# Kernel optimization log

Measured on AMD Instinct MI355X. Metric: run time of the kernel, lower is better.

The kernel has to match this reference:

```python
import jax, jax.numpy as jnp
import numpy as np

N_GAUSS = 1536
WIDTH, HEIGHT = 160, 128
FX = FY = 146.44        # 2343.024 * (160/2560)
CX, CY = WIDTH / 2.0, HEIGHT / 2.0
EPS2D = 0.3             # 2D covariance dilation (as in prepare_rasterization_coefficients)
NEAR, FAR = 0.01, 1e10


def eval_sh_basis(dirs):
    # real SH basis up to degree 3, 16 components (matches eval_sh_old)
    x, y, z = dirs[..., 0], dirs[..., 1], dirs[..., 2]
    one = jnp.ones_like(x)
    return jnp.stack([
        0.282095 * one,
        -0.488603 * y, 0.488603 * z, -0.488603 * x,
        1.092548 * x * y, -1.092548 * y * z, 0.315392 * (3 * z * z - 1),
        -1.092548 * x * z, 0.546274 * (x * x - y * y),
        -0.590044 * y * (3 * x * x - y * y), 2.890611 * x * y * z,
        -0.457046 * y * (5 * z * z - 1), 0.373176 * z * (5 * z * z - 3),
        -0.457046 * x * (5 * z * z - 1), 1.445306 * z * (x * x - y * y),
        -0.590044 * x * (x * x - 3 * y * y)], axis=-1)


def quat_to_rot(q):
    q = q / jnp.linalg.norm(q, axis=1, keepdims=True)
    w, x, y, z = q[:, 0], q[:, 1], q[:, 2], q[:, 3]
    R = jnp.stack([
        1 - 2 * (y * y + z * z), 2 * (x * y - z * w), 2 * (x * z + y * w),
        2 * (x * y + z * w), 1 - 2 * (x * x + z * z), 2 * (y * z - x * w),
        2 * (x * z - y * w), 2 * (y * z + x * w), 1 - 2 * (x * x + y * y)], axis=-1)
    return R.reshape(-1, 3, 3)


def get_viewmat(c2w):
    # c2w: (B,3,4); flip y/z camera axes then invert (matches torch get_viewmat)
    R = c2w[:, :3, :3] * jnp.array([[[1.0, -1.0, -1.0]]], dtype=c2w.dtype)
    t = c2w[:, :3, 3:4]
    R_inv = jnp.swapaxes(R, 1, 2)
    t_inv = -(R_inv @ t)
    return R_inv[0], t_inv[0, :, 0]


def setup_inputs() -> dict:
    key = jax.random.key(0)
    k0, k1, k2, k3, k4, k5 = jax.random.split(key, 6)
    N = N_GAUSS
    xy = jax.random.normal(k0, (N, 2), dtype=jnp.float32) * 0.5
    # world z negative -> positive camera-frame depth after axis flip
    z = -(1.0 + 4.0 * jax.random.uniform(k1, (N, 1), dtype=jnp.float32))
    means = jnp.concatenate([xy, z], axis=1)
    quats = jax.random.normal(k2, (N, 4), dtype=jnp.float32)
    log_scales = jax.random.normal(k3, (N, 3), dtype=jnp.float32) * 0.3 - 3.0
    opacity_logits = jax.random.normal(k4, (N,), dtype=jnp.float32)
    sh_coeffs = jax.random.normal(k5, (N, 16, 3), dtype=jnp.float32) * 0.3
    camera_to_worlds = jnp.eye(4, dtype=jnp.float32)[None, :3, :]
    return {"means": means, "quats": quats, "log_scales": log_scales,
            "opacity_logits": opacity_logits, "sh_coeffs": sh_coeffs,
            "camera_to_worlds": camera_to_worlds}


def reference(means, quats, log_scales, opacity_logits, sh_coeffs, camera_to_worlds):
    R_w2c, t_w2c = get_viewmat(camera_to_worlds)
    means_cam = means @ R_w2c.T + t_w2c                    # (N,3)
    depth = means_cam[:, 2]
    mask = (depth > NEAR) & (depth < FAR)

    # view-dependent colors from SH (degree 3)
    cam_pos = camera_to_worlds[0, :3, 3]
    dirs = means - cam_pos
    dirs = dirs / jnp.linalg.norm(dirs, axis=1, keepdims=True)
    colors = jnp.maximum(jnp.einsum('nk,nkc->nc', eval_sh_basis(dirs), sh_coeffs) + 0.5, 0.0)

    # 3D covariance -> camera frame -> EWA 2D projection
    Rg = quat_to_rot(quats)                                 # (N,3,3)
    M = Rg * jnp.exp(log_scales)[:, None, :]                # R @ diag(S)
    cov3d = M @ jnp.swapaxes(M, 1, 2)
    cov_cam = jnp.einsum('ij,njk,lk->nil', R_w2c, cov3d, R_w2c)
    tx, ty, tz = means_cam[:, 0], means_cam[:, 1], means_cam[:, 2]
    rz = 1.0 / tz
    zero = jnp.zeros_like(rz)
    J = jnp.stack([jnp.stack([FX * rz, zero, -FX * tx * rz * rz], -1),
                   jnp.stack([zero, FY * rz, -FY * ty * rz * rz], -1)], -2)  # (N,2,3)
    cov2d = jnp.einsum('nij,njk,nlk->nil', J, cov_cam, J)
    a = cov2d[:, 0, 0] + EPS2D
    c = cov2d[:, 1, 1] + EPS2D
    b = cov2d[:, 0, 1]
    det = a * c - b * b
    A, B, C = c / det, -b / det, a / det                    # conic (inverse 2D cov)

    u = FX * tx * rz + CX
    v = FY * ty * rz + CY
    opac = jax.nn.sigmoid(opacity_logits)

    px = jnp.arange(WIDTH, dtype=means.dtype)
    py = jnp.arange(HEIGHT, dtype=means.dtype)
    dx = px[None, None, :] - u[:, None, None]               # (N,1,W)
    dy = py[None, :, None] - v[:, None, None]               # (N,H,1)
    power = (-0.5 * (A[:, None, None] * dx * dx + C[:, None, None] * dy * dy)
             - B[:, None, None] * (dx * dy))                # (N,H,W)
    alpha = jnp.minimum(0.999, opac[:, None, None] * jnp.exp(power))
    alpha = jnp.where(mask[:, None, None], alpha, 0.0)

    # global depth sort (front-to-back alpha compositing)
    order = jnp.argsort(jnp.where(mask, depth, jnp.inf))
    alpha = alpha[order]
    colors = colors[order]
    T = jnp.cumprod(1.0 - alpha, axis=0)
    T_excl = jnp.concatenate([jnp.ones_like(T[:1]), T[:-1]], axis=0)
    w = T_excl * alpha                                      # (N,H,W)
    rgb = jnp.einsum('nhw,nc->hwc', w, colors)              # (H,W,3)
    return rgb
```

## Files before the change

### kernel.cpp

```cpp
#include <hip/hip_runtime.h>
#include <math.h>

#define N_GAUSS 1536
#define WIDTH   160
#define HEIGHT  128
#define NPIX    (WIDTH * HEIGHT)
#define FXC     146.44f
#define FYC     146.44f
#define CXC     80.0f
#define CYC     64.0f
#define EPS2D   0.3f
#define NEARP   0.01f
#define FARP    1e10f
#define REC     12
#define L2E     1.4426950408889634f

#define PREP_BLOCKS 384
#define PREP_TPB    256
#define SCAN_LEN4   (N_GAUSS / 64 / 4)

#define NWAVE   16
#define RCHUNK  (N_GAUSS / NWAVE)
#define RPIX    64

__device__ __forceinline__ float fast_exp2(float x) {
    return __builtin_amdgcn_exp2f(x);
}


__global__ __launch_bounds__(PREP_TPB) void prep_sort_kernel(
    const float* __restrict__ means, const float* __restrict__ quats,
    const float* __restrict__ log_scales, const float* __restrict__ opac_logits,
    const float* __restrict__ sh, const float* __restrict__ c2w,
    float* __restrict__ sorted)
{
    __shared__ float4 k4_lds[N_GAUSS / 4];
    float* k_lds = (float*)k4_lds;

    float C[12];
#pragma unroll
    for (int k = 0; k < 12; k++) C[k] = c2w[k];
    float R00 =  C[0], R01 =  C[4], R02 =  C[8];
    float R10 = -C[1], R11 = -C[5], R12 = -C[9];
    float R20 = -C[2], R21 = -C[6], R22 = -C[10];
    float cpx = C[3], cpy = C[7], cpz = C[11];
    float t0 = -(R00 * cpx + R01 * cpy + R02 * cpz);
    float t1 = -(R10 * cpx + R11 * cpy + R12 * cpz);
    float t2 = -(R20 * cpx + R21 * cpy + R22 * cpz);

    for (int j = threadIdx.x; j < N_GAUSS; j += PREP_TPB) {
        float mx = means[3 * j], my = means[3 * j + 1], mz = means[3 * j + 2];
        float tzj = R20 * mx + R21 * my + R22 * mz + t2;
        bool m = (tzj > NEARP) && (tzj < FARP);
        k_lds[j] = m ? tzj : INFINITY;
    }
    __syncthreads();

    int i    = blockIdx.x * 4 + (threadIdx.x >> 6);
    int part = threadIdx.x & 63;

    float mx = means[3 * i], my = means[3 * i + 1], mz = means[3 * i + 2];
    float4 qv = ((const float4*)quats)[i];
    float lsx = log_scales[3 * i + 0];
    float lsy = log_scales[3 * i + 1];
    float lsz = log_scales[3 * i + 2];
    float olog = opac_logits[i];
    const float4* sh4 = (const float4*)(sh + i * 48);
    float4 S[12];
#pragma unroll
    for (int k = 0; k < 12; k++) S[k] = sh4[k];
    const float* shf = (const float*)S;

    float tx = R00 * mx + R01 * my + R02 * mz + t0;
    float ty = R10 * mx + R11 * my + R12 * mz + t1;
    float tz = R20 * mx + R21 * my + R22 * mz + t2;
    bool mask = (tz > NEARP) && (tz < FARP);

    float dx = mx - cpx, dy = my - cpy, dz = mz - cpz;
    float rn = rsqrtf(dx * dx + dy * dy + dz * dz);
    float x = dx * rn, y = dy * rn, z = dz * rn;
    float xx = x * x, yy = y * y, zz = z * z;
    float basis[16];
    basis[0]  = 0.282095f;
    basis[1]  = -0.488603f * y;
    basis[2]  = 0.488603f * z;
    basis[3]  = -0.488603f * x;
    basis[4]  = 1.092548f * x * y;
    basis[5]  = -1.092548f * y * z;
    basis[6]  = 0.315392f * (3.f * zz - 1.f);
    basis[7]  = -1.092548f * x * z;
    basis[8]  = 0.546274f * (xx - yy);
    basis[9]  = -0.590044f * y * (3.f * xx - yy);
    basis[10] = 2.890611f * x * y * z;
    basis[11] = -0.457046f * y * (5.f * zz - 1.f);
    basis[12] = 0.373176f * z * (5.f * zz - 3.f);
    basis[13] = -0.457046f * x * (5.f * zz - 1.f);
    basis[14] = 1.445306f * z * (xx - yy);
    basis[15] = -0.590044f * x * (xx - 3.f * yy);
    float cr = 0.f, cg = 0.f, cb = 0.f;
#pragma unroll
    for (int k = 0; k < 16; k++) {
        cr += basis[k] * shf[3 * k + 0];
        cg += basis[k] * shf[3 * k + 1];
        cb += basis[k] * shf[3 * k + 2];
    }
    cr = fmaxf(cr + 0.5f, 0.f);
    cg = fmaxf(cg + 0.5f, 0.f);
    cb = fmaxf(cb + 0.5f, 0.f);

    float qw = qv.x, qx = qv.y, qy = qv.z, qz = qv.w;
    float qn = rsqrtf(qw * qw + qx * qx + qy * qy + qz * qz);
    qw *= qn; qx *= qn; qy *= qn; qz *= qn;
    float sx = expf(lsx);
    float sy = expf(lsy);
    float sz = expf(lsz);
    float M00 = (1.f - 2.f * (qy * qy + qz * qz)) * sx;
    float M01 = (2.f * (qx * qy - qz * qw)) * sy;
    float M02 = (2.f * (qx * qz + qy * qw)) * sz;
    float M10 = (2.f * (qx * qy + qz * qw)) * sx;
    float M11 = (1.f - 2.f * (qx * qx + qz * qz)) * sy;
    float M12 = (2.f * (qy * qz - qx * qw)) * sz;
    float M20 = (2.f * (qx * qz - qy * qw)) * sx;
    float M21 = (2.f * (qy * qz + qx * qw)) * sy;
    float M22 = (1.f - 2.f * (qx * qx + qy * qy)) * sz;
    float V00 = M00 * M00 + M01 * M01 + M02 * M02;
    float V01 = M00 * M10 + M01 * M11 + M02 * M12;
    float V02 = M00 * M20 + M01 * M21 + M02 * M22;
    float V11 = M10 * M10 + M11 * M11 + M12 * M12;
    float V12 = M10 * M20 + M11 * M21 + M12 * M22;
    float V22 = M20 * M20 + M21 * M21 + M22 * M22;

    float T00 = R00 * V00 + R01 * V01 + R02 * V02;
    float T01 = R00 * V01 + R01 * V11 + R02 * V12;
    float T02 = R00 * V02 + R01 * V12 + R02 * V22;
    float T10 = R10 * V00 + R11 * V01 + R12 * V02;
    float T11 = R10 * V01 + R11 * V11 + R12 * V12;
    float T12 = R10 * V02 + R11 * V12 + R12 * V22;
    float T20 = R20 * V00 + R21 * V01 + R22 * V02;
    float T21 = R20 * V01 + R21 * V11 + R22 * V12;
    float T22 = R20 * V02 + R21 * V12 + R22 * V22;
    float cc00 = T00 * R00 + T01 * R01 + T02 * R02;
    float cc01 = T00 * R10 + T01 * R11 + T02 * R12;
    float cc02 = T00 * R20 + T01 * R21 + T02 * R22;
    float cc11 = T10 * R10 + T11 * R11 + T12 * R12;
    float cc12 = T10 * R20 + T11 * R21 + T12 * R22;
    float cc22 = T20 * R20 + T21 * R21 + T22 * R22;

    float rz = 1.f / tz;
    float rz2 = rz * rz;
    float j00 = FXC * rz, j02 = -FXC * tx * rz2;
    float j11 = FYC * rz, j12 = -FYC * ty * rz2;
    float c2d00 = j00 * j00 * cc00 + 2.f * j00 * j02 * cc02 + j02 * j02 * cc22;
    float c2d01 = (j00 * cc01 + j02 * cc12) * j11 + (j00 * cc02 + j02 * cc22) * j12;
    float c2d11 = j11 * j11 * cc11 + 2.f * j11 * j12 * cc12 + j12 * j12 * cc22;

    float a = c2d00 + EPS2D, c = c2d11 + EPS2D, b = c2d01;
    float idet = 1.f / (a * c - b * b);
    float Ac = c * idet, Bc = -b * idet, Cc = a * idet;
    float u = FXC * tx * rz + CXC;
    float v = FYC * ty * rz + CYC;
    float op = 1.f / (1.f + expf(-olog));
    float a2 = -0.5f * L2E * Ac;
    float b2 = -L2E * Bc;
    float c2 = -0.5f * L2E * Cc;
    float o2 = log2f(op);
    if (!mask) {
        u = 0.f; v = 0.f; a2 = 0.f; b2 = 0.f; c2 = 0.f; o2 = -INFINITY;
    }

    float ki = k_lds[i];
    int rank = 0;
    int base4 = part * SCAN_LEN4;
#pragma unroll
    for (int jj = 0; jj < SCAN_LEN4; jj++) {
        int j4 = base4 + jj;
        float4 kk = k4_lds[j4];
        int j = 4 * j4;
        rank += (kk.x < ki) || (kk.x == ki && (j + 0) < i);
        rank += (kk.y < ki) || (kk.y == ki && (j + 1) < i);
        rank += (kk.z < ki) || (kk.z == ki && (j + 2) < i);
        rank += (kk.w < ki) || (kk.w == ki && (j + 3) < i);
    }
    rank += __shfl_xor(rank, 1);
    rank += __shfl_xor(rank, 2);
    rank += __shfl_xor(rank, 4);
    rank += __shfl_xor(rank, 8);
    rank += __shfl_xor(rank, 16);
    rank += __shfl_xor(rank, 32);

    if (part == 0) {
        float4* dst = (float4*)(sorted + rank * REC);
        dst[0] = make_float4(u, v, a2, b2);
        dst[1] = make_float4(c2, o2, cr, cg);
        dst[2] = make_float4(cb, 0.f, 0.f, 0.f);
    }
}

__global__ __launch_bounds__(1024) void raster_kernel(
    const float4* __restrict__ sorted4, float* __restrict__ out)
{
    __shared__ float4 part_lds[NWAVE * RPIX];

    int wave = __builtin_amdgcn_readfirstlane(threadIdx.x >> 6);
    int lane = threadIdx.x & 63;
    int p = blockIdx.x * RPIX + lane;
    float px = (float)(p % WIDTH);
    float py = (float)(p / WIDTH);

    const float4* src = sorted4 + wave * (RCHUNK * 3);

    float T = 1.f, cr = 0.f, cg = 0.f, cb = 0.f;
#pragma unroll 4
    for (int j = 0; j < RCHUNK; j++) {
        float4 f0 = src[3 * j + 0];
        float4 f1 = src[3 * j + 1];
        float4 f2 = src[3 * j + 2];
        float dx = px - f0.x;
        float dy = py - f0.y;
        float t  = f0.z * dx;
        t = fmaf(f0.w, dy, t);
        float q  = f1.x * dy;
        float pw = fmaf(t, dx, f1.y);
        pw = fmaf(q, dy, pw);
        float alpha = fminf(0.999f, fast_exp2(pw));
        float w = T * alpha;
        cr = fmaf(w, f1.z, cr);
        cg = fmaf(w, f1.w, cg);
        cb = fmaf(w, f2.x, cb);
        T -= w;
    }
    part_lds[wave * RPIX + lane] = make_float4(cr, cg, cb, T);
    __syncthreads();

    if (threadIdx.x < RPIX) {
        int pp = blockIdx.x * RPIX + threadIdx.x;
        float Tt = 1.f, r = 0.f, g = 0.f, b = 0.f;
#pragma unroll
        for (int c = 0; c < NWAVE; c++) {
            float4 q = part_lds[c * RPIX + threadIdx.x];
            r = fmaf(Tt, q.x, r);
            g = fmaf(Tt, q.y, g);
            b = fmaf(Tt, q.z, b);
            Tt *= q.w;
        }
        out[3 * pp + 0] = r;
        out[3 * pp + 1] = g;
        out[3 * pp + 2] = b;
    }
}

extern "C" void kernel_launch(void* const* d_in, const int* in_sizes, int n_in,
                              void* d_out, int out_size, void* d_ws, size_t ws_size,
                              hipStream_t stream) {
    const float* means       = (const float*)d_in[0];
    const float* quats       = (const float*)d_in[1];
    const float* log_scales  = (const float*)d_in[2];
    const float* opac_logits = (const float*)d_in[3];
    const float* sh          = (const float*)d_in[4];
    const float* c2w         = (const float*)d_in[5];

    float* ws     = (float*)d_ws;
    float* sorted = ws;

    prep_sort_kernel<<<PREP_BLOCKS, PREP_TPB, 0, stream>>>(
        means, quats, log_scales, opac_logits, sh, c2w, sorted);
    raster_kernel<<<NPIX / RPIX, NWAVE * 64, 0, stream>>>(
        (const float4*)sorted, (float*)d_out);
}
```

Baseline: 87.90 us.

## Cull Gaussians per 8x8 tile using screen-space bounding boxes

The prep kernel now emits a per-Gaussian bounding box (center plus radii at which the opacity-weighted Gaussian falls below exp(-25)) alongside a reorganized record layout. The raster kernel switches from linear 64-pixel strips to 8x8 tiles. Each wave ballots which of its Gaussians overlap the tile and only evaluates those, skipping the exp and blend for distant splats. This drops contributions below the exp(-25) cutoff, which is a small approximation to the reference. It also adds ballot/shuffle overhead and divergent loop trip counts.

```diff
diff --git a/kernel.cpp b/kernel.cpp
--- a/kernel.cpp
+++ b/kernel.cpp
@@ -12,8 +12,9 @@
 #define EPS2D   0.3f
 #define NEARP   0.01f
 #define FARP    1e10f
-#define REC     12
 #define L2E     1.4426950408889634f
+#define LN2     0.6931471805599453f
+#define CULL_E  25.0f
 
 #define PREP_BLOCKS 384
 #define PREP_TPB    256
@@ -22,6 +23,10 @@
 #define NWAVE   16
 #define RCHUNK  (N_GAUSS / NWAVE)
 #define RPIX    64
+#define TILE_W  8
+#define TILE_H  8
+#define TILES_X (WIDTH / TILE_W)
+#define TILES_Y (HEIGHT / TILE_H)
 
 __device__ __forceinline__ float fast_exp2(float x) {
     return __builtin_amdgcn_exp2f(x);
@@ -32,7 +37,7 @@
     const float* __restrict__ means, const float* __restrict__ quats,
     const float* __restrict__ log_scales, const float* __restrict__ opac_logits,
     const float* __restrict__ sh, const float* __restrict__ c2w,
-    float* __restrict__ sorted)
+    float4* __restrict__ bbox, float4* __restrict__ rec)
 {
     __shared__ float4 k4_lds[N_GAUSS / 4];
     float* k_lds = (float*)k4_lds;
@@ -164,8 +169,14 @@
     float b2 = -L2E * Bc;
     float c2 = -0.5f * L2E * Cc;
     float o2 = log2f(op);
+
+    float Qmax = fmaxf(0.f, 2.f * LN2 * (CULL_E + o2));
+    float rx = sqrtf(Qmax * a);
+    float ry = sqrtf(Qmax * c);
+
     if (!mask) {
-        u = 0.f; v = 0.f; a2 = 0.f; b2 = 0.f; c2 = 0.f; o2 = -INFINITY;
+        u = 1e30f; v = 1e30f; rx = 0.f; ry = 0.f;
+        a2 = 0.f; b2 = 0.f; c2 = 0.f; o2 = -INFINITY;
     }
 
     float ki = k_lds[i];
@@ -189,63 +200,82 @@
     rank += __shfl_xor(rank, 32);
 
     if (part == 0) {
-        float4* dst = (float4*)(sorted + rank * REC);
-        dst[0] = make_float4(u, v, a2, b2);
-        dst[1] = make_float4(c2, o2, cr, cg);
-        dst[2] = make_float4(cb, 0.f, 0.f, 0.f);
+        bbox[rank]        = make_float4(u, v, rx, ry);
+        rec[2 * rank]     = make_float4(a2, b2, c2, o2);
+        rec[2 * rank + 1] = make_float4(cr, cg, cb, 0.f);
     }
 }
 
 __global__ __launch_bounds__(1024) void raster_kernel(
-    const float4* __restrict__ sorted4, float* __restrict__ out)
+    const float4* __restrict__ bbox, const float4* __restrict__ rec,
+    float* __restrict__ out)
 {
     __shared__ float4 part_lds[NWAVE * RPIX];
 
     int wave = __builtin_amdgcn_readfirstlane(threadIdx.x >> 6);
     int lane = threadIdx.x & 63;
-    int p = blockIdx.x * RPIX + lane;
-    float px = (float)(p % WIDTH);
-    float py = (float)(p / WIDTH);
-
-    const float4* src = sorted4 + wave * (RCHUNK * 3);
+
+    int tile = blockIdx.x;
+    int tx0 = (tile % TILES_X) * TILE_W;
+    int ty0 = (tile / TILES_X) * TILE_H;
+    float px = (float)(tx0 + (lane & 7));
+    float py = (float)(ty0 + (lane >> 3));
+    float tcx = (float)tx0 + 3.5f;
+    float tcy = (float)ty0 + 3.5f;
+
+    int g0 = wave * RCHUNK;
 
     float T = 1.f, cr = 0.f, cg = 0.f, cb = 0.f;
-#pragma unroll 4
-    for (int j = 0; j < RCHUNK; j++) {
-        float4 f0 = src[3 * j + 0];
-        float4 f1 = src[3 * j + 1];
-        float4 f2 = src[3 * j + 2];
-        float dx = px - f0.x;
-        float dy = py - f0.y;
-        float t  = f0.z * dx;
-        t = fmaf(f0.w, dy, t);
-        float q  = f1.x * dy;
-        float pw = fmaf(t, dx, f1.y);
-        pw = fmaf(q, dy, pw);
-        float alpha = fminf(0.999f, fast_exp2(pw));
-        float w = T * alpha;
-        cr = fmaf(w, f1.z, cr);
-        cg = fmaf(w, f1.w, cg);
-        cb = fmaf(w, f2.x, cb);
-        T -= w;
+#pragma unroll
+    for (int bseg = 0; bseg < 2; bseg++) {
+        int gbase = g0 + (bseg ? 64 : 0);
+        int bn    = bseg ? 32 : 64;
+        float4 bb = bbox[gbase + (lane < bn ? lane : 0)];
+        bool ok = (lane < bn) &&
+                  (fabsf(tcx - bb.x) <= bb.z + 3.5f) &&
+                  (fabsf(tcy - bb.y) <= bb.w + 3.5f);
+        unsigned long long m = __ballot(ok);
+        while (m) {
+            int bl = __ffsll(m) - 1;
+            m &= m - 1;
+            float u = __shfl(bb.x, bl);
+            float v = __shfl(bb.y, bl);
+            int g = gbase + bl;
+            float4 f1 = rec[2 * g];
+            float4 f2 = rec[2 * g + 1];
+            float dx = px - u;
+            float dy = py - v;
+            float t  = f1.x * dx;
+            t = fmaf(f1.y, dy, t);
+            float q  = f1.z * dy;
+            float pw = fmaf(t, dx, f1.w);
+            pw = fmaf(q, dy, pw);
+            float alpha = fminf(0.999f, fast_exp2(pw));
+            float w = T * alpha;
+            cr = fmaf(w, f2.x, cr);
+            cg = fmaf(w, f2.y, cg);
+            cb = fmaf(w, f2.z, cb);
+            T -= w;
+        }
     }
     part_lds[wave * RPIX + lane] = make_float4(cr, cg, cb, T);
     __syncthreads();
 
     if (threadIdx.x < RPIX) {
-        int pp = blockIdx.x * RPIX + threadIdx.x;
+        int l = threadIdx.x;
+        int p = (ty0 + (l >> 3)) * WIDTH + tx0 + (l & 7);
         float Tt = 1.f, r = 0.f, g = 0.f, b = 0.f;
 #pragma unroll
         for (int c = 0; c < NWAVE; c++) {
-            float4 q = part_lds[c * RPIX + threadIdx.x];
+            float4 q = part_lds[c * RPIX + l];
             r = fmaf(Tt, q.x, r);
             g = fmaf(Tt, q.y, g);
             b = fmaf(Tt, q.z, b);
             Tt *= q.w;
         }
-        out[3 * pp + 0] = r;
-        out[3 * pp + 1] = g;
-        out[3 * pp + 2] = b;
+        out[3 * p + 0] = r;
+        out[3 * p + 1] = g;
+        out[3 * p + 2] = b;
     }
 }
 
@@ -259,11 +289,12 @@
     const float* sh          = (const float*)d_in[4];
     const float* c2w         = (const float*)d_in[5];
 
-    float* ws     = (float*)d_ws;
-    float* sorted = ws;
+    float* ws = (float*)d_ws;
+    float4* bbox = (float4*)ws;
+    float4* rec  = (float4*)(ws + N_GAUSS * 4);
 
     prep_sort_kernel<<<PREP_BLOCKS, PREP_TPB, 0, stream>>>(
-        means, quats, log_scales, opac_logits, sh, c2w, sorted);
-    raster_kernel<<<NPIX / RPIX, NWAVE * 64, 0, stream>>>(
-        (const float4*)sorted, (float*)d_out);
+        means, quats, log_scales, opac_logits, sh, c2w, bbox, rec);
+    raster_kernel<<<TILES_X * TILES_Y, NWAVE * 64, 0, stream>>>(
+        bbox, rec, (float*)d_out);
 }
```

New measurement: 78.12 us (median of 2 runs). -11.1%, faster.
